# Kernel tuning notes

Hardware: AMD Instinct MI355X
Metric: run time of the kernel (lower is better)

The kernel has to match this reference:

```python
import jax, jax.numpy as jnp
import numpy as np
import math

DIM = 2048
N_HEADS = 32
N_KV_HEADS = 8
HEAD_DIM = DIM // N_HEADS  # 64
N_REP = N_HEADS // N_KV_HEADS  # 4
BSZ = 2
SEQLEN = 2048
ROPE_THETA = 10000.0


def setup_inputs() -> dict:
    key = jax.random.key(0)
    k_x, k_q, k_k, k_v, k_o = jax.random.split(key, 5)
    x = jax.random.normal(k_x, (BSZ, SEQLEN, DIM), dtype=jnp.float32)
    scale = 0.02
    wq = jax.random.normal(k_q, (N_HEADS * HEAD_DIM, DIM), dtype=jnp.float32) * scale
    wk = jax.random.normal(k_k, (N_KV_HEADS * HEAD_DIM, DIM), dtype=jnp.float32) * scale
    wv = jax.random.normal(k_v, (N_KV_HEADS * HEAD_DIM, DIM), dtype=jnp.float32) * scale
    wo = jax.random.normal(k_o, (DIM, N_HEADS * HEAD_DIM), dtype=jnp.float32) * scale
    # RoPE frequencies: freqs_cis = exp(i * t * theta^{-2j/d}), j in [0, d/2)
    inv_freq = 1.0 / (ROPE_THETA ** (np.arange(0, HEAD_DIM, 2, dtype=np.float32) / HEAD_DIM))
    t = np.arange(SEQLEN, dtype=np.float32)
    freqs = np.outer(t, inv_freq)  # [S, HEAD_DIM//2]
    freqs_cos = jnp.asarray(np.cos(freqs), dtype=jnp.float32)
    freqs_sin = jnp.asarray(np.sin(freqs), dtype=jnp.float32)
    # causal additive mask [1,1,S,S]
    neg_inf = jnp.finfo(jnp.float32).min
    mask = jnp.where(jnp.tril(jnp.ones((SEQLEN, SEQLEN), dtype=bool)), 0.0, neg_inf)
    mask = mask[None, None, :, :].astype(jnp.float32)
    return {"x": x, "freqs_cos": freqs_cos, "freqs_sin": freqs_sin, "mask": mask,
            "wq": wq, "wk": wk, "wv": wv, "wo": wo}


def _apply_rotary(xq, xk, cos, sin):
    # xq: [B,S,H,D], xk: [B,S,Hkv,D]; cos/sin: [S, D//2]
    def rot(t):
        tr = t.reshape(*t.shape[:-1], -1, 2)  # [..., D//2, 2]
        tr_r, tr_i = tr[..., 0], tr[..., 1]
        c = cos[None, :, None, :]
        s = sin[None, :, None, :]
        out_r = tr_r * c - tr_i * s
        out_i = tr_r * s + tr_i * c
        return jnp.stack([out_r, out_i], axis=-1).reshape(t.shape)
    return rot(xq), rot(xk)


def reference(x, freqs_cos, freqs_sin, mask, wq, wk, wv, wo):
    bsz, seqlen, _ = x.shape
    xq = jnp.einsum('bsd,ed->bse', x, wq).reshape(bsz, seqlen, N_HEADS, HEAD_DIM)
    xk = jnp.einsum('bsd,ed->bse', x, wk).reshape(bsz, seqlen, N_KV_HEADS, HEAD_DIM)
    xv = jnp.einsum('bsd,ed->bse', x, wv).reshape(bsz, seqlen, N_KV_HEADS, HEAD_DIM)
    xq, xk = _apply_rotary(xq, xk, freqs_cos, freqs_sin)
    # GQA: repeat_interleave kv heads
    xk = jnp.repeat(xk, N_REP, axis=2)  # [B,S,H,D]
    xv = jnp.repeat(xv, N_REP, axis=2)
    # [B,H,S,D]
    q = xq.transpose(0, 2, 1, 3)
    k = xk.transpose(0, 2, 1, 3)
    v = xv.transpose(0, 2, 1, 3)
    scores = jnp.einsum('bhqd,bhkd->bhqk', q, k) / math.sqrt(HEAD_DIM)
    scores = scores + mask
    probs = jax.nn.softmax(scores.astype(jnp.float32), axis=-1).astype(q.dtype)
    out = jnp.einsum('bhqk,bhkd->bhqd', probs, v)
    out = out.transpose(0, 2, 1, 3).reshape(bsz, seqlen, N_HEADS * HEAD_DIM)
    return jnp.einsum('bse,de->bsd', out, wo)
```

## Files before the change

### kernel.cpp

```cpp
#include <hip/hip_runtime.h>
#include <hip/hip_bf16.h>
#include <stdint.h>

typedef __bf16 bf16x8 __attribute__((ext_vector_type(8)));
typedef float f32x4 __attribute__((ext_vector_type(4)));
typedef unsigned short u16;
typedef u16 u16x8 __attribute__((ext_vector_type(8)));

__device__ __forceinline__ float bf2f(u16 u) {
  union { uint32_t i; float f; } v; v.i = uint32_t(u) << 16; return v.f;
}
__device__ __forceinline__ u16 f2bf(float f) {
  union { float f; uint32_t i; } v; v.f = f;
  uint32_t r = v.i + 0x7FFFu + ((v.i >> 16) & 1u);
  return (u16)(r >> 16);
}
__device__ __forceinline__ uint32_t pack2(float a, float b) {
  union { __bf16 h[2]; uint32_t u; } v;
  v.h[0] = (__bf16)a; v.h[1] = (__bf16)b; return v.u;
}
__device__ __forceinline__ float exp2x(float x) { return __builtin_amdgcn_exp2f(x); }
__device__ __forceinline__ float max3f(float a, float b, float c) {
  return fmaxf(fmaxf(a, b), c);
}

typedef __attribute__((address_space(1))) const uint32_t gas_u32;
typedef __attribute__((address_space(3))) uint32_t las_u32;
__device__ __forceinline__ void gload_lds16(const u16* g, u16* l) {
  __builtin_amdgcn_global_load_lds((gas_u32*)g, (las_u32*)l, 16, 0, 0);
}

#define QSCL 0.180336880111f

__global__ __launch_bounds__(256) void conv4(
    const float* __restrict__ x, const float* __restrict__ wq,
    const float* __restrict__ wk, const float* __restrict__ wv,
    u16* __restrict__ Xb, u16* __restrict__ Wqb,
    u16* __restrict__ Wkb, u16* __restrict__ Wvb)
{
  int t = blockIdx.x * 256 + threadIdx.x;
  const float* src; u16* dst;
  if (t < 1048576)      { src = x;  dst = Xb; }
  else if (t < 1572864) { src = wq; dst = Wqb; t -= 1048576; }
  else if (t < 1703936) { src = wk; dst = Wkb; t -= 1572864; }
  else                  { src = wv; dst = Wvb; t -= 1703936; }
  const int i = t * 8;
  const float4 a = *reinterpret_cast<const float4*>(src + i);
  const float4 b = *reinterpret_cast<const float4*>(src + i + 4);
  u16x8 o;
  o[0] = f2bf(a.x); o[1] = f2bf(a.y); o[2] = f2bf(a.z); o[3] = f2bf(a.w);
  o[4] = f2bf(b.x); o[5] = f2bf(b.y); o[6] = f2bf(b.z); o[7] = f2bf(b.w);
  *reinterpret_cast<u16x8*>(dst + i) = o;
}

__global__ __launch_bounds__(256) void f32_to_bf16(
    const float* __restrict__ in, u16* __restrict__ out, int n)
{
  const int i = (blockIdx.x * 256 + threadIdx.x) * 8;
  if (i >= n) return;
  const float4 a = *reinterpret_cast<const float4*>(in + i);
  const float4 b = *reinterpret_cast<const float4*>(in + i + 4);
  u16x8 o;
  o[0] = f2bf(a.x); o[1] = f2bf(a.y); o[2] = f2bf(a.z); o[3] = f2bf(a.w);
  o[4] = f2bf(b.x); o[5] = f2bf(b.y); o[6] = f2bf(b.z); o[7] = f2bf(b.w);
  *reinterpret_cast<u16x8*>(out + i) = o;
}

__device__ __forceinline__ void gemm_core(
    const u16* __restrict__ A, const u16* __restrict__ Bw,
    int row0, int col0, int K,
    u16* As, u16* Bs, f32x4 acc[4][4])
{
  const int tid = threadIdx.x, wv = tid >> 6, lane = tid & 63;
  const int l15 = lane & 15, lhi = lane >> 4;
  const int wr = (wv >> 1) * 64, wc = (wv & 1) * 64;

  int srow[4], scol[4], ldso[4];
#pragma unroll
  for (int sh = 0; sh < 4; ++sh) {
    const int idx = sh * 256 + tid;
    srow[sh] = idx >> 3;
    scol[sh] = ((idx & 7) ^ (srow[sh] & 7)) * 8;
    ldso[sh] = (sh * 256 + wv * 64) * 8;
  }

  for (int k0 = 0; k0 < K; k0 += 64) {
#pragma unroll
    for (int sh = 0; sh < 4; ++sh)
      gload_lds16(A + (size_t)(row0 + srow[sh]) * K + k0 + scol[sh], As + ldso[sh]);
#pragma unroll
    for (int sh = 0; sh < 4; ++sh)
      gload_lds16(Bw + (size_t)(col0 + srow[sh]) * K + k0 + scol[sh], Bs + ldso[sh]);
    __syncthreads();

#pragma unroll
    for (int kc = 0; kc < 2; ++kc) {
      bf16x8 af[4], bfv[4];
#pragma unroll
      for (int i = 0; i < 4; ++i) {
        const int ra = wr + i * 16 + l15;
        af[i] = *reinterpret_cast<const bf16x8*>(
            reinterpret_cast<const char*>(As) +
            ((ra * 128 + kc * 64 + lhi * 16) ^ ((ra & 7) << 4)));
        const int rb = wc + i * 16 + l15;
        bfv[i] = *reinterpret_cast<const bf16x8*>(
            reinterpret_cast<const char*>(Bs) +
            ((rb * 128 + kc * 64 + lhi * 16) ^ ((rb & 7) << 4)));
      }
#pragma unroll
      for (int mi = 0; mi < 4; ++mi)
#pragma unroll
        for (int ni = 0; ni < 4; ++ni)
          acc[mi][ni] = __builtin_amdgcn_mfma_f32_16x16x32_bf16(af[mi], bfv[ni], acc[mi][ni], 0, 0, 0);
    }
    __syncthreads();
  }
}

template <int F32OUT, int ROPE>
__global__ __launch_bounds__(256) void gemm_bt2(
    const u16* __restrict__ A, const u16* __restrict__ Bw, void* __restrict__ Cv,
    int N, int K, int ldc,
    const float* __restrict__ cosb, const float* __restrict__ sinb)
{
  __shared__ u16 As[128 * 64];
  __shared__ u16 Bs[128 * 64];
  const int nwg = gridDim.x * gridDim.y;
  int lin = blockIdx.y * gridDim.x + blockIdx.x;
  lin = (lin & 7) * (nwg >> 3) + (lin >> 3);
  const int row0 = (lin / gridDim.x) * 128, col0 = (lin % gridDim.x) * 128;
  f32x4 acc[4][4] = {};
  gemm_core(A, Bw, row0, col0, K, As, Bs, acc);

  const int lane = threadIdx.x & 63, wv = threadIdx.x >> 6;
  const int wr = (wv >> 1) * 64, wc = (wv & 1) * 64;
  const int l15 = lane & 15;
#pragma unroll
  for (int mi = 0; mi < 4; ++mi) {
    const int r0 = row0 + wr + mi * 16 + ((lane >> 4) << 2);
#pragma unroll
    for (int ni = 0; ni < 4; ++ni) {
      const int c = col0 + wc + ni * 16 + l15;
#pragma unroll
      for (int r = 0; r < 4; ++r) {
        if (ROPE) {
          const int s = (r0 + r) & 2047;
          const int jj = (c & 63) >> 1;
          const float cvv = cosb[s * 32 + jj], svv = sinb[s * 32 + jj];
          const float val = acc[mi][ni][r];
          const float part = __shfl_xor(val, 1);
          const float sgn = (c & 1) ? svv : -svv;
          reinterpret_cast<u16*>(Cv)[(size_t)(r0 + r) * ldc + c] =
              f2bf((val * cvv + part * sgn) * QSCL);
        } else if (F32OUT) {
          reinterpret_cast<float*>(Cv)[(size_t)(r0 + r) * ldc + c] = acc[mi][ni][r];
        } else {
          reinterpret_cast<u16*>(Cv)[(size_t)(r0 + r) * ldc + c] = f2bf(acc[mi][ni][r]);
        }
      }
    }
  }
}

__global__ __launch_bounds__(256) void gemm_kv(
    const u16* __restrict__ A, const u16* __restrict__ Wk, const u16* __restrict__ Wv,
    u16* __restrict__ Kout, u16* __restrict__ VTout, int K,
    const float* __restrict__ cosb, const float* __restrict__ sinb)
{
  __shared__ u16 As[128 * 64];
  __shared__ u16 Bs[128 * 64];
  int lin = blockIdx.y * 8 + blockIdx.x;
  lin = (lin & 7) * 32 + (lin >> 3);
  const int bx = lin & 7, by = lin >> 3;
  const bool isV = bx >= 4;
  const int col0 = (bx & 3) * 128;
  const int row0 = by * 128;
  f32x4 acc[4][4] = {};
  gemm_core(A, isV ? Wv : Wk, row0, col0, K, As, Bs, acc);

  const int lane = threadIdx.x & 63, wv = threadIdx.x >> 6;
  const int wr = (wv >> 1) * 64, wc = (wv & 1) * 64;
  const int l15 = lane & 15;
#pragma unroll
  for (int mi = 0; mi < 4; ++mi) {
    const int r0 = row0 + wr + mi * 16 + ((lane >> 4) << 2);
#pragma unroll
    for (int ni = 0; ni < 4; ++ni) {
      const int c = col0 + wc + ni * 16 + l15;
#pragma unroll
      for (int r = 0; r < 4; ++r) {
        if (isV) {
          VTout[(size_t)c * 4096 + (r0 + r)] = f2bf(acc[mi][ni][r]);
        } else {
          const int s = (r0 + r) & 2047;
          const int jj = (c & 63) >> 1;
          const float cvv = cosb[s * 32 + jj], svv = sinb[s * 32 + jj];
          const float val = acc[mi][ni][r];
          const float part = __shfl_xor(val, 1);
          const float sgn = (c & 1) ? svv : -svv;
          Kout[(size_t)(r0 + r) * 512 + c] = f2bf(val * cvv + part * sgn);
        }
      }
    }
  }
}

__device__ __forceinline__ bf16x8 lds_read8(const u16* base, int row, int col) {
  const int byte = (row * 128 + col * 2) ^ ((row & 7) << 4);
  return *reinterpret_cast<const bf16x8*>(reinterpret_cast<const char*>(base) + byte);
}
__device__ __forceinline__ void lds_write4(u16* base, int row, int col, uint32_t v) {
  const int byte = (row * 128 + col * 2) ^ ((row & 7) << 4);
  *reinterpret_cast<uint32_t*>(reinterpret_cast<char*>(base) + byte) = v;
}

__device__ __forceinline__ void attn_set(
    const u16* __restrict__ Ks, const u16* __restrict__ Vt, u16* __restrict__ Plw,
    const bf16x8 qf[2], const bf16x8 ones, int t0, int qbase, int l15, int lhi,
    float& mrun, f32x4& lrun, f32x4 oacc[4])
{
  f32x4 s[4] = {};
#pragma unroll
  for (int kc = 0; kc < 2; ++kc)
#pragma unroll
    for (int f = 0; f < 4; ++f) {
      const bf16x8 kf = lds_read8(Ks, f * 16 + l15, kc * 32 + lhi * 8);
      s[f] = __builtin_amdgcn_mfma_f32_16x16x32_bf16(kf, qf[kc], s[f], 0, 0, 0);
    }
  float v[4][4];
#pragma unroll
  for (int f = 0; f < 4; ++f)
#pragma unroll
    for (int r = 0; r < 4; ++r) v[f][r] = s[f][r];
  if (t0 + 63 > qbase) {
#pragma unroll
    for (int f = 0; f < 4; ++f)
#pragma unroll
      for (int r = 0; r < 4; ++r)
        if (t0 + f * 16 + lhi * 4 + r > qbase + l15) v[f][r] = -1e30f;
  }
  float t1 = max3f(v[0][0], v[0][1], v[0][2]);
  float t2 = max3f(v[0][3], v[1][0], v[1][1]);
  float t3 = max3f(v[1][2], v[1][3], v[2][0]);
  float t4 = max3f(v[2][1], v[2][2], v[2][3]);
  float t5 = max3f(v[3][0], v[3][1], v[3][2]);
  float mx = fmaxf(max3f(t1, t2, t3), max3f(t4, t5, v[3][3]));
  mx = fmaxf(mx, __shfl_xor(mx, 16));
  mx = fmaxf(mx, __shfl_xor(mx, 32));
  if (!__all(mx <= mrun + 8.f)) {
    const float newm = fmaxf(mrun, mx);
    const float fac = exp2x(mrun - newm);
    mrun = newm;
    float facq[4];
#pragma unroll
    for (int r = 0; r < 4; ++r) facq[r] = __shfl(fac, lhi * 4 + r);
#pragma unroll
    for (int r = 0; r < 4; ++r) lrun[r] *= facq[r];
#pragma unroll
    for (int nf = 0; nf < 4; ++nf)
#pragma unroll
      for (int r = 0; r < 4; ++r) oacc[nf][r] *= facq[r];
  }
#pragma unroll
  for (int f = 0; f < 4; ++f) {
    const float p0 = exp2x(v[f][0] - mrun), p1 = exp2x(v[f][1] - mrun);
    const float p2 = exp2x(v[f][2] - mrun), p3 = exp2x(v[f][3] - mrun);
    lds_write4(Plw, l15, f * 16 + lhi * 4,     pack2(p0, p1));
    lds_write4(Plw, l15, f * 16 + lhi * 4 + 2, pack2(p2, p3));
  }
#pragma unroll
  for (int kc = 0; kc < 2; ++kc) {
    const bf16x8 pa = lds_read8(Plw, l15, kc * 32 + lhi * 8);
    lrun = __builtin_amdgcn_mfma_f32_16x16x32_bf16(pa, ones, lrun, 0, 0, 0);
#pragma unroll
    for (int nf = 0; nf < 4; ++nf) {
      const bf16x8 vf = lds_read8(Vt, nf * 16 + l15, kc * 32 + lhi * 8);
      oacc[nf] = __builtin_amdgcn_mfma_f32_16x16x32_bf16(pa, vf, oacc[nf], 0, 0, 0);
    }
  }
}

__device__ __forceinline__ void attn_store(
    u16* __restrict__ O, const size_t qoff, const int h, const int qbase,
    const int l15, const int lhi, const f32x4 lrun, const f32x4 oacc[4])
{
  float linv[4];
#pragma unroll
  for (int r = 0; r < 4; ++r) linv[r] = 1.f / lrun[r];
#pragma unroll
  for (int nf = 0; nf < 4; ++nf)
#pragma unroll
    for (int r = 0; r < 4; ++r)
      O[qoff + (size_t)(qbase + lhi * 4 + r) * 2048 + h * 64 + nf * 16 + l15] =
          f2bf(oacc[nf][r] * linv[r]);
}

__global__ __launch_bounds__(256) void attn_kernel(
    const u16* __restrict__ Q, const u16* __restrict__ K,
    const u16* __restrict__ VT, u16* __restrict__ O)
{
  __shared__ u16 Ks[2][64 * 64];
  __shared__ u16 Vt[2][64 * 64];
  __shared__ u16 Pl[4][16 * 64];

  const int j  = blockIdx.x;
  const int h  = blockIdx.y;
  const int b  = blockIdx.z;
  const int kh = h >> 2;
  const int tid = threadIdx.x, wv = tid >> 6, lane = tid & 63;
  const int l15 = lane & 15, lhi = lane >> 4;
  const size_t qoff = (size_t)b * 2048 * 2048;
  const size_t koff = (size_t)b * 2048 * 512;

  const int qAb = j * 64 + wv * 16;
  const int qBb = (31 - j) * 64 + wv * 16;

  const int idx0 = tid, idx1 = tid + 256;
  const int r0 = idx0 >> 3, u0 = (idx0 & 7) ^ (r0 & 7);
  const int r1 = idx1 >> 3, u1 = (idx1 & 7) ^ (r1 & 7);
  const u16* const kg0 = K + koff + (size_t)r0 * 512 + kh * 64 + u0 * 8;
  const u16* const kg1 = K + koff + (size_t)r1 * 512 + kh * 64 + u1 * 8;
  const u16* const vg0 = VT + (size_t)(kh * 64 + r0) * 4096 + b * 2048 + u0 * 8;
  const u16* const vg1 = VT + (size_t)(kh * 64 + r1) * 4096 + b * 2048 + u1 * 8;
  const int ld0 = wv * 512;
  const int ld1 = 2048 + wv * 512;

  bf16x8 qfA[2], qfB[2];
#pragma unroll
  for (int kc = 0; kc < 2; ++kc) {
    qfA[kc] = *reinterpret_cast<const bf16x8*>(
        Q + qoff + (size_t)(qAb + l15) * 2048 + h * 64 + kc * 32 + lhi * 8);
    qfB[kc] = *reinterpret_cast<const bf16x8*>(
        Q + qoff + (size_t)(qBb + l15) * 2048 + h * 64 + kc * 32 + lhi * 8);
  }
  bf16x8 ones;
#pragma unroll
  for (int i = 0; i < 8; ++i) ones[i] = (__bf16)1.0f;

  float mA = -1e30f, mB = -1e30f;
  f32x4 lA = {}, lB = {};
  f32x4 oA[4] = {}, oB[4] = {};

  const int tlast = 31 - j;

  gload_lds16(kg0, &Ks[0][ld0]);
  gload_lds16(kg1, &Ks[0][ld1]);
  gload_lds16(vg0, &Vt[0][ld0]);
  gload_lds16(vg1, &Vt[0][ld1]);
  __syncthreads();

  int cur = 0;
  for (int t = 0; t <= tlast; ++t) {
    const int t0 = t * 64;
    if (t < tlast) {
      const int n0 = t0 + 64;
      const int nb = cur ^ 1;
      gload_lds16(kg0 + (size_t)n0 * 512, &Ks[nb][ld0]);
      gload_lds16(kg1 + (size_t)n0 * 512, &Ks[nb][ld1]);
      gload_lds16(vg0 + n0, &Vt[nb][ld0]);
      gload_lds16(vg1 + n0, &Vt[nb][ld1]);
    }

    if (t <= j)
      attn_set(Ks[cur], Vt[cur], Pl[wv], qfA, ones, t0, qAb, l15, lhi, mA, lA, oA);
    attn_set(Ks[cur], Vt[cur], Pl[wv], qfB, ones, t0, qBb, l15, lhi, mB, lB, oB);

    __syncthreads();
    cur ^= 1;
  }

  attn_store(O, qoff, h, qAb, l15, lhi, lA, oA);
  attn_store(O, qoff, h, qBb, l15, lhi, lB, oB);
}

extern "C" void kernel_launch(void* const* d_in, const int* in_sizes, int n_in,
                              void* d_out, int out_size, void* d_ws, size_t ws_size,
                              hipStream_t stream)
{
  const float* x  = (const float*)d_in[0];
  const float* fc = (const float*)d_in[1];
  const float* fs = (const float*)d_in[2];
  const float* wq = (const float*)d_in[4];
  const float* wk = (const float*)d_in[5];
  const float* wv = (const float*)d_in[6];
  const float* wo = (const float*)d_in[7];
  float* out = (float*)d_out;

  u16* Xb  = (u16*)d_ws;
  u16* Wqb = Xb  + (size_t)4096 * 2048;
  u16* Wkb = Wqb + (size_t)2048 * 2048;
  u16* Wvb = Wkb + (size_t)512 * 2048;
  u16* Qws = Wvb + (size_t)512 * 2048;
  u16* Kws = Qws + (size_t)4096 * 2048;
  u16* VTws = Kws + (size_t)4096 * 512;
  u16* Ows = Xb;
  u16* Wob = Wqb;

  dim3 blk(256);
  conv4<<<dim3((1048576 + 524288 + 131072 + 131072) / 256), blk, 0, stream>>>(
      x, wq, wk, wv, Xb, Wqb, Wkb, Wvb);
  gemm_bt2<0,1><<<dim3(16, 32), blk, 0, stream>>>(Xb, Wqb, Qws, 2048, 2048, 2048, fc, fs);
  gemm_kv<<<dim3(8, 32), blk, 0, stream>>>(Xb, Wkb, Wvb, Kws, VTws, 2048, fc, fs);
  f32_to_bf16<<<dim3(2048 * 2048 / 8 / 256), blk, 0, stream>>>(wo, Wob, 2048 * 2048);
  attn_kernel<<<dim3(16, 32, 2), blk, 0, stream>>>(Qws, Kws, VTws, Ows);
  gemm_bt2<1,0><<<dim3(16, 32), blk, 0, stream>>>(Ows, Wob, out, 2048, 2048, 2048, nullptr, nullptr);
}
```

Measured before the change: 265.9 us.

## Merge Q and KV projection launches, fold Wo conversion, raise MFMA priority in attention

Combines the Q projection and the K/V projection into a single 768-block launch, so the smaller KV GEMM no longer runs as a separate under-filled wave after the Q GEMM. Folds the Wo fp32-to-bf16 conversion into the initial conversion kernel, which needs a dedicated workspace slot for Wo instead of reusing the Wq buffer. Also wraps the MFMA sections of the attention inner loop in s_setprio raises so matrix work gets issue priority over softmax code from other waves. Net effect: two fewer kernel launches and better CU occupancy during projection, at the cost of extra workspace memory.

```diff
diff --git a/kernel.cpp b/kernel.cpp
--- a/kernel.cpp
+++ b/kernel.cpp
@@ -32,18 +32,20 @@
 
 #define QSCL 0.180336880111f
 
-__global__ __launch_bounds__(256) void conv4(
+__global__ __launch_bounds__(256) void conv5(
     const float* __restrict__ x, const float* __restrict__ wq,
     const float* __restrict__ wk, const float* __restrict__ wv,
+    const float* __restrict__ wo,
     u16* __restrict__ Xb, u16* __restrict__ Wqb,
-    u16* __restrict__ Wkb, u16* __restrict__ Wvb)
+    u16* __restrict__ Wkb, u16* __restrict__ Wvb, u16* __restrict__ Wob)
 {
   int t = blockIdx.x * 256 + threadIdx.x;
   const float* src; u16* dst;
   if (t < 1048576)      { src = x;  dst = Xb; }
   else if (t < 1572864) { src = wq; dst = Wqb; t -= 1048576; }
   else if (t < 1703936) { src = wk; dst = Wkb; t -= 1572864; }
-  else                  { src = wv; dst = Wvb; t -= 1703936; }
+  else if (t < 1835008) { src = wv; dst = Wvb; t -= 1703936; }
+  else                  { src = wo; dst = Wob; t -= 1835008; }
   const int i = t * 8;
   const float4 a = *reinterpret_cast<const float4*>(src + i);
   const float4 b = *reinterpret_cast<const float4*>(src + i + 4);
@@ -51,19 +53,6 @@
   o[0] = f2bf(a.x); o[1] = f2bf(a.y); o[2] = f2bf(a.z); o[3] = f2bf(a.w);
   o[4] = f2bf(b.x); o[5] = f2bf(b.y); o[6] = f2bf(b.z); o[7] = f2bf(b.w);
   *reinterpret_cast<u16x8*>(dst + i) = o;
-}
-
-__global__ __launch_bounds__(256) void f32_to_bf16(
-    const float* __restrict__ in, u16* __restrict__ out, int n)
-{
-  const int i = (blockIdx.x * 256 + threadIdx.x) * 8;
-  if (i >= n) return;
-  const float4 a = *reinterpret_cast<const float4*>(in + i);
-  const float4 b = *reinterpret_cast<const float4*>(in + i + 4);
-  u16x8 o;
-  o[0] = f2bf(a.x); o[1] = f2bf(a.y); o[2] = f2bf(a.z); o[3] = f2bf(a.w);
-  o[4] = f2bf(b.x); o[5] = f2bf(b.y); o[6] = f2bf(b.z); o[7] = f2bf(b.w);
-  *reinterpret_cast<u16x8*>(out + i) = o;
 }
 
 __device__ __forceinline__ void gemm_core(
@@ -117,11 +106,77 @@
   }
 }
 
-template <int F32OUT, int ROPE>
-__global__ __launch_bounds__(256) void gemm_bt2(
-    const u16* __restrict__ A, const u16* __restrict__ Bw, void* __restrict__ Cv,
-    int N, int K, int ldc,
+__global__ __launch_bounds__(256) void gemm_qkv(
+    const u16* __restrict__ A, const u16* __restrict__ Wq,
+    const u16* __restrict__ Wk, const u16* __restrict__ Wv,
+    u16* __restrict__ Qout, u16* __restrict__ Kout, u16* __restrict__ VTout,
     const float* __restrict__ cosb, const float* __restrict__ sinb)
+{
+  __shared__ u16 As[128 * 64];
+  __shared__ u16 Bs[128 * 64];
+  int lin = blockIdx.x;
+  lin = (lin & 7) * 96 + (lin >> 3);
+  const int lane = threadIdx.x & 63, wvi = threadIdx.x >> 6;
+  const int wr = (wvi >> 1) * 64, wc = (wvi & 1) * 64;
+  const int l15 = lane & 15;
+  f32x4 acc[4][4] = {};
+
+  if (lin < 512) {
+    const int row0 = (lin >> 4) * 128, col0 = (lin & 15) * 128;
+    gemm_core(A, Wq, row0, col0, 2048, As, Bs, acc);
+#pragma unroll
+    for (int mi = 0; mi < 4; ++mi) {
+      const int r0 = row0 + wr + mi * 16 + ((lane >> 4) << 2);
+#pragma unroll
+      for (int ni = 0; ni < 4; ++ni) {
+        const int c = col0 + wc + ni * 16 + l15;
+#pragma unroll
+        for (int r = 0; r < 4; ++r) {
+          const int s = (r0 + r) & 2047;
+          const int jj = (c & 63) >> 1;
+          const float cvv = cosb[s * 32 + jj], svv = sinb[s * 32 + jj];
+          const float val = acc[mi][ni][r];
+          const float part = __shfl_xor(val, 1);
+          const float sgn = (c & 1) ? svv : -svv;
+          Qout[(size_t)(r0 + r) * 2048 + c] = f2bf((val * cvv + part * sgn) * QSCL);
+        }
+      }
+    }
+  } else {
+    const int t = lin - 512;
+    const int bx = t & 7, by = t >> 3;
+    const bool isV = bx >= 4;
+    const int col0 = (bx & 3) * 128;
+    const int row0 = by * 128;
+    gemm_core(A, isV ? Wv : Wk, row0, col0, 2048, As, Bs, acc);
+#pragma unroll
+    for (int mi = 0; mi < 4; ++mi) {
+      const int r0 = row0 + wr + mi * 16 + ((lane >> 4) << 2);
+#pragma unroll
+      for (int ni = 0; ni < 4; ++ni) {
+        const int c = col0 + wc + ni * 16 + l15;
+#pragma unroll
+        for (int r = 0; r < 4; ++r) {
+          if (isV) {
+            VTout[(size_t)c * 4096 + (r0 + r)] = f2bf(acc[mi][ni][r]);
+          } else {
+            const int s = (r0 + r) & 2047;
+            const int jj = (c & 63) >> 1;
+            const float cvv = cosb[s * 32 + jj], svv = sinb[s * 32 + jj];
+            const float val = acc[mi][ni][r];
+            const float part = __shfl_xor(val, 1);
+            const float sgn = (c & 1) ? svv : -svv;
+            Kout[(size_t)(r0 + r) * 512 + c] = f2bf(val * cvv + part * sgn);
+          }
+        }
+      }
+    }
+  }
+}
+
+__global__ __launch_bounds__(256) void gemm_out(
+    const u16* __restrict__ A, const u16* __restrict__ Bw, float* __restrict__ C,
+    int N, int K)
 {
   __shared__ u16 As[128 * 64];
   __shared__ u16 Bs[128 * 64];
@@ -132,8 +187,8 @@
   f32x4 acc[4][4] = {};
   gemm_core(A, Bw, row0, col0, K, As, Bs, acc);
 
-  const int lane = threadIdx.x & 63, wv = threadIdx.x >> 6;
-  const int wr = (wv >> 1) * 64, wc = (wv & 1) * 64;
+  const int lane = threadIdx.x & 63, wvi = threadIdx.x >> 6;
+  const int wr = (wvi >> 1) * 64, wc = (wvi & 1) * 64;
   const int l15 = lane & 15;
 #pragma unroll
   for (int mi = 0; mi < 4; ++mi) {
@@ -142,65 +197,8 @@
     for (int ni = 0; ni < 4; ++ni) {
       const int c = col0 + wc + ni * 16 + l15;
 #pragma unroll
-      for (int r = 0; r < 4; ++r) {
-        if (ROPE) {
-          const int s = (r0 + r) & 2047;
-          const int jj = (c & 63) >> 1;
-          const float cvv = cosb[s * 32 + jj], svv = sinb[s * 32 + jj];
-          const float val = acc[mi][ni][r];
-          const float part = __shfl_xor(val, 1);
-          const float sgn = (c & 1) ? svv : -svv;
-          reinterpret_cast<u16*>(Cv)[(size_t)(r0 + r) * ldc + c] =
-              f2bf((val * cvv + part * sgn) * QSCL);
-        } else if (F32OUT) {
-          reinterpret_cast<float*>(Cv)[(size_t)(r0 + r) * ldc + c] = acc[mi][ni][r];
-        } else {
-          reinterpret_cast<u16*>(Cv)[(size_t)(r0 + r) * ldc + c] = f2bf(acc[mi][ni][r]);
-        }
-      }
-    }
-  }
-}
-
-__global__ __launch_bounds__(256) void gemm_kv(
-    const u16* __restrict__ A, const u16* __restrict__ Wk, const u16* __restrict__ Wv,
-    u16* __restrict__ Kout, u16* __restrict__ VTout, int K,
-    const float* __restrict__ cosb, const float* __restrict__ sinb)
-{
-  __shared__ u16 As[128 * 64];
-  __shared__ u16 Bs[128 * 64];
-  int lin = blockIdx.y * 8 + blockIdx.x;
-  lin = (lin & 7) * 32 + (lin >> 3);
-  const int bx = lin & 7, by = lin >> 3;
-  const bool isV = bx >= 4;
-  const int col0 = (bx & 3) * 128;
-  const int row0 = by * 128;
-  f32x4 acc[4][4] = {};
-  gemm_core(A, isV ? Wv : Wk, row0, col0, K, As, Bs, acc);
-
-  const int lane = threadIdx.x & 63, wv = threadIdx.x >> 6;
-  const int wr = (wv >> 1) * 64, wc = (wv & 1) * 64;
-  const int l15 = lane & 15;
-#pragma unroll
-  for (int mi = 0; mi < 4; ++mi) {
-    const int r0 = row0 + wr + mi * 16 + ((lane >> 4) << 2);
-#pragma unroll
-    for (int ni = 0; ni < 4; ++ni) {
-      const int c = col0 + wc + ni * 16 + l15;
-#pragma unroll
-      for (int r = 0; r < 4; ++r) {
-        if (isV) {
-          VTout[(size_t)c * 4096 + (r0 + r)] = f2bf(acc[mi][ni][r]);
-        } else {
-          const int s = (r0 + r) & 2047;
-          const int jj = (c & 63) >> 1;
-          const float cvv = cosb[s * 32 + jj], svv = sinb[s * 32 + jj];
-          const float val = acc[mi][ni][r];
-          const float part = __shfl_xor(val, 1);
-          const float sgn = (c & 1) ? svv : -svv;
-          Kout[(size_t)(r0 + r) * 512 + c] = f2bf(val * cvv + part * sgn);
-        }
-      }
+      for (int r = 0; r < 4; ++r)
+        C[(size_t)(r0 + r) * N + c] = acc[mi][ni][r];
     }
   }
 }
@@ -220,6 +218,7 @@
     float& mrun, f32x4& lrun, f32x4 oacc[4])
 {
   f32x4 s[4] = {};
+  __builtin_amdgcn_s_setprio(1);
 #pragma unroll
   for (int kc = 0; kc < 2; ++kc)
 #pragma unroll
@@ -227,6 +226,7 @@
       const bf16x8 kf = lds_read8(Ks, f * 16 + l15, kc * 32 + lhi * 8);
       s[f] = __builtin_amdgcn_mfma_f32_16x16x32_bf16(kf, qf[kc], s[f], 0, 0, 0);
     }
+  __builtin_amdgcn_s_setprio(0);
   float v[4][4];
 #pragma unroll
   for (int f = 0; f < 4; ++f)
@@ -268,6 +268,7 @@
     lds_write4(Plw, l15, f * 16 + lhi * 4,     pack2(p0, p1));
     lds_write4(Plw, l15, f * 16 + lhi * 4 + 2, pack2(p2, p3));
   }
+  __builtin_amdgcn_s_setprio(1);
 #pragma unroll
   for (int kc = 0; kc < 2; ++kc) {
     const bf16x8 pa = lds_read8(Plw, l15, kc * 32 + lhi * 8);
@@ -278,6 +279,7 @@
       oacc[nf] = __builtin_amdgcn_mfma_f32_16x16x32_bf16(pa, vf, oacc[nf], 0, 0, 0);
     }
   }
+  __builtin_amdgcn_s_setprio(0);
 }
 
 __device__ __forceinline__ void attn_store(
@@ -393,15 +395,13 @@
   u16* Qws = Wvb + (size_t)512 * 2048;
   u16* Kws = Qws + (size_t)4096 * 2048;
   u16* VTws = Kws + (size_t)4096 * 512;
+  u16* Wob = VTws + (size_t)512 * 4096;
   u16* Ows = Xb;
-  u16* Wob = Wqb;
 
   dim3 blk(256);
-  conv4<<<dim3((1048576 + 524288 + 131072 + 131072) / 256), blk, 0, stream>>>(
-      x, wq, wk, wv, Xb, Wqb, Wkb, Wvb);
-  gemm_bt2<0,1><<<dim3(16, 32), blk, 0, stream>>>(Xb, Wqb, Qws, 2048, 2048, 2048, fc, fs);
-  gemm_kv<<<dim3(8, 32), blk, 0, stream>>>(Xb, Wkb, Wvb, Kws, VTws, 2048, fc, fs);
-  f32_to_bf16<<<dim3(2048 * 2048 / 8 / 256), blk, 0, stream>>>(wo, Wob, 2048 * 2048);
+  conv5<<<dim3(2359296 / 256), blk, 0, stream>>>(
+      x, wq, wk, wv, wo, Xb, Wqb, Wkb, Wvb, Wob);
+  gemm_qkv<<<dim3(768), blk, 0, stream>>>(Xb, Wqb, Wkb, Wvb, Qws, Kws, VTws, fc, fs);
   attn_kernel<<<dim3(16, 32, 2), blk, 0, stream>>>(Qws, Kws, VTws, Ows);
-  gemm_bt2<1,0><<<dim3(16, 32), blk, 0, stream>>>(Ows, Wob, out, 2048, 2048, 2048, nullptr, nullptr);
-}
+  gemm_out<<<dim3(16, 32), blk, 0, stream>>>(Ows, Wob, out, 2048, 2048);
+}
```

Result: no change. 267.5 us (+0.6%).
